# Performance work log

Hardware: AMD Instinct MI355X
Metric: run time of the kernel (lower is better)

The kernel has to match this reference:

```python
import jax, jax.numpy as jnp
import numpy as np

N_GENES = 2000
D_MODEL = 256
N_LAYERS = 4
D_STATE = 16
D_CONV = 4
EXPAND = 2
D_INNER = EXPAND * D_MODEL  # 512
DT_RANK = (D_MODEL + 15) // 16  # 16


def layer_norm(x, w, b, eps=1e-5):
    mu = jnp.mean(x, axis=-1, keepdims=True)
    var = jnp.mean((x - mu) ** 2, axis=-1, keepdims=True)
    return (x - mu) * jax.lax.rsqrt(var + eps) * w + b


def mamba_mixer(h, in_w, cw, cb, xp_w, dtp_w, dtp_b, A_log, Dvec, out_w):
    # h: [B, L, d_model]
    B, L, _ = h.shape
    xz = jnp.einsum('bld,ed->ble', h, in_w)            # [B,L,2*Di]
    u, z = jnp.split(xz, 2, axis=-1)                    # [B,L,Di] each
    # causal depthwise conv1d (kernel D_CONV)
    up = jnp.pad(u, ((0, 0), (D_CONV - 1, 0), (0, 0)))
    u = sum(up[:, k:k + L, :] * cw[:, k] for k in range(D_CONV)) + cb
    u = jax.nn.silu(u)
    # input-dependent dt, B, C
    xdbc = jnp.einsum('bld,ed->ble', u, xp_w)           # [B,L,dt_rank+2N]
    dt_r = xdbc[..., :DT_RANK]
    Bm = xdbc[..., DT_RANK:DT_RANK + D_STATE]           # [B,L,N]
    Cm = xdbc[..., DT_RANK + D_STATE:]                  # [B,L,N]
    dt = jax.nn.softplus(jnp.einsum('blr,dr->bld', dt_r, dtp_w) + dtp_b)  # [B,L,Di]
    A = -jnp.exp(A_log)                                 # [Di,N]
    dA = jnp.exp(dt[..., None] * A)                     # [B,L,Di,N]
    dBu = dt[..., None] * Bm[:, :, None, :] * u[..., None]

    def step(hst, inp):
        a, bu = inp
        hst = a * hst + bu
        return hst, hst

    h0 = jnp.zeros((B, D_INNER, D_STATE), dA.dtype)
    _, hs = jax.lax.scan(step, h0, (jnp.moveaxis(dA, 1, 0), jnp.moveaxis(dBu, 1, 0)))
    y = jnp.einsum('lbdn,lbn->bld', hs, jnp.moveaxis(Cm, 1, 0)) + u * Dvec
    y = y * jax.nn.silu(z)
    return jnp.einsum('bld,ed->ble', y, out_w)          # [B,L,d_model]


def setup_inputs() -> dict:
    key = jax.random.key(0)
    ks = jax.random.split(key, 16)
    nl = N_LAYERS
    inp = {
        'x': jax.random.normal(ks[0], (2, N_GENES), jnp.float32),
        'bulk_in_w': jax.random.normal(ks[1], (D_MODEL,), jnp.float32),
        'bulk_in_b': jnp.zeros((D_MODEL,), jnp.float32),
        'gene_emb': jax.random.normal(ks[2], (1, N_GENES, D_MODEL), jnp.float32) * 0.02,
        'mod_emb': jax.random.normal(ks[3], (1, 1, D_MODEL), jnp.float32) * 0.02,
        'ln_w': jnp.ones((nl, D_MODEL), jnp.float32),
        'ln_b': jnp.zeros((nl, D_MODEL), jnp.float32),
        'in_proj_w': jax.random.normal(ks[4], (nl, 2 * D_INNER, D_MODEL), jnp.float32) * (D_MODEL ** -0.5),
        'conv_w': jax.random.normal(ks[5], (nl, D_INNER, D_CONV), jnp.float32) * (D_CONV ** -0.5),
        'conv_b': jnp.zeros((nl, D_INNER), jnp.float32),
        'x_proj_w': jax.random.normal(ks[6], (nl, DT_RANK + 2 * D_STATE, D_INNER), jnp.float32) * (D_INNER ** -0.5),
        'dt_proj_w': jax.random.normal(ks[7], (nl, D_INNER, DT_RANK), jnp.float32) * 0.01,
        'dt_proj_b': jnp.full((nl, D_INNER), -4.0, jnp.float32),
        'A_log': jnp.broadcast_to(jnp.log(jnp.arange(1, D_STATE + 1, dtype=jnp.float32)), (nl, D_INNER, D_STATE)).copy(),
        'D': jnp.ones((nl, D_INNER), jnp.float32),
        'out_proj_w': jax.random.normal(ks[8], (nl, D_MODEL, D_INNER), jnp.float32) * (D_INNER ** -0.5),
        'fin_w': jnp.ones((D_MODEL,), jnp.float32),
        'fin_b': jnp.zeros((D_MODEL,), jnp.float32),
        'head_w': jax.random.normal(ks[9], (D_MODEL,), jnp.float32) * (D_MODEL ** -0.5),
        'head_b': jnp.zeros((), jnp.float32),
    }
    return inp


def reference(x, bulk_in_w, bulk_in_b, gene_emb, mod_emb, ln_w, ln_b, in_proj_w,
              conv_w, conv_b, x_proj_w, dt_proj_w, dt_proj_b, A_log, D, out_proj_w,
              fin_w, fin_b, head_w, head_b):
    # token embed (modality='bulk'); Linear(1,d_model) == x[...,None]*w + b
    h = x[..., None] * bulk_in_w + bulk_in_b + gene_emb + mod_emb  # [B,L,d_model]
    for i in range(N_LAYERS):
        h = h + mamba_mixer(layer_norm(h, ln_w[i], ln_b[i]), in_proj_w[i], conv_w[i],
                            conv_b[i], x_proj_w[i], dt_proj_w[i], dt_proj_b[i],
                            A_log[i], D[i], out_proj_w[i])
    h = layer_norm(h, fin_w, fin_b)
    y = jnp.einsum('bld,d->bl', h, head_w) + head_b  # bulk head, squeeze(-1)
    return y
```

## Files before the change

kernel.cpp:

```cpp
#include <hip/hip_runtime.h>
#include <math.h>

#define B_  2
#define L_  2000
#define DM_ 256
#define DI_ 512
#define DS_ 16
#define NL_ 4
#define BL_ (B_*L_)
#define BLP_ 4096
#define NC_  125
#define CL_  16
#define NST_ (B_*DI_*DS_)

#define NF_IP_ (NL_*64*8*64)
#define NF_OP_ (NL_*16*16*64)
#define NF_XP_ (NL_*3*16*64)
#define NF_TOT_ (NF_IP_ + NF_OP_ + NF_XP_)

typedef unsigned short ushort_t;
typedef __attribute__((ext_vector_type(8))) short bf16x8;
typedef __attribute__((ext_vector_type(4))) float f32x4;

__device__ __forceinline__ float siluf(float x) { return x / (1.f + __expf(-x)); }
__device__ __forceinline__ ushort_t f2bf(float x) {
    unsigned int u = __float_as_uint(x);
    return (ushort_t)((u + 0x7FFFu + ((u >> 16) & 1u)) >> 16);
}
__device__ __forceinline__ float bf2f(ushort_t v) {
    return __uint_as_float(((unsigned int)v) << 16);
}

__global__ __launch_bounds__(256) void embed_f2bf_kernel(
    const float* __restrict__ x, const float* __restrict__ biw,
    const float* __restrict__ bib, const float* __restrict__ ge,
    const float* __restrict__ me, const float* __restrict__ lnw,
    const float* __restrict__ lnb,
    float* __restrict__ h, ushort_t* __restrict__ aln,
    const float* __restrict__ ipw, const float* __restrict__ opw,
    const float* __restrict__ xpw, ushort_t* __restrict__ ipwb,
    ushort_t* __restrict__ opwb, ushort_t* __restrict__ xpwb)
{
    if (blockIdx.x < BL_) {
        __shared__ float sm[8];
        int bl = blockIdx.x, d = threadIdx.x;
        int l = bl % L_;
        float v = x[bl]*biw[d] + bib[d] + ge[(size_t)l*DM_ + d] + me[d];
        h[(size_t)bl*DM_ + d] = v;
        float s = v, q = v*v;
        #pragma unroll
        for (int o = 32; o > 0; o >>= 1) {
            s += __shfl_down(s, o);
            q += __shfl_down(q, o);
        }
        if ((d & 63) == 0) { sm[d >> 6] = s; sm[4 + (d >> 6)] = q; }
        __syncthreads();
        float sum = sm[0]+sm[1]+sm[2]+sm[3];
        float ssq = sm[4]+sm[5]+sm[6]+sm[7];
        float mu  = sum * (1.f/DM_);
        float inv = rsqrtf(fmaxf(ssq*(1.f/DM_) - mu*mu, 0.f) + 1e-5f);
        aln[(size_t)bl*DM_ + d] = f2bf((v - mu)*inv*lnw[d] + lnb[d]);
    } else {
        int i = (blockIdx.x - BL_)*256 + threadIdx.x;
        if (i >= NF_TOT_) return;
        const float* src; ushort_t* dst;
        if (i < NF_IP_) {
            int f = i;
            int li   = f >> 15;
            int r    = f & 32767;
            int t    = r >> 9;
            int rem  = r & 511;
            int ks   = rem >> 6;
            int lane = rem & 63;
            src = ipw + ((size_t)(li*1024 + t*16 + (lane & 15)))*DM_
                      + ks*32 + (lane >> 4)*8;
            dst = ipwb + (size_t)f*8;
        } else if (i < NF_IP_ + NF_OP_) {
            int f = i - NF_IP_;
            int li   = f >> 14;
            int r    = f & 16383;
            int t    = r >> 10;
            int rem  = r & 1023;
            int ks   = rem >> 6;
            int lane = rem & 63;
            src = opw + ((size_t)(li*256 + t*16 + (lane & 15)))*DI_
                      + ks*32 + (lane >> 4)*8;
            dst = opwb + (size_t)f*8;
        } else {
            int f = i - NF_IP_ - NF_OP_;
            int li   = f / 3072;
            int r    = f % 3072;
            int t    = r >> 10;
            int rem  = r & 1023;
            int ks   = rem >> 6;
            int lane = rem & 63;
            src = xpw + ((size_t)(li*48 + t*16 + (lane & 15)))*DI_
                      + ks*32 + (lane >> 4)*8;
            dst = xpwb + (size_t)f*8;
        }
        float4 v0 = *(const float4*)src;
        float4 v1 = *(const float4*)(src + 4);
        __align__(16) ushort_t o[8];
        o[0] = f2bf(v0.x); o[1] = f2bf(v0.y); o[2] = f2bf(v0.z); o[3] = f2bf(v0.w);
        o[4] = f2bf(v1.x); o[5] = f2bf(v1.y); o[6] = f2bf(v1.z); o[7] = f2bf(v1.w);
        *(uint4*)dst = *(const uint4*)o;
    }
}

__global__ __launch_bounds__(256) void gemm_bf(
    const ushort_t* __restrict__ A, const ushort_t* __restrict__ Wp,
    ushort_t* __restrict__ C)
{
    __shared__ ushort_t a_s[128*64];
    const int r0 = blockIdx.x*128, c0 = blockIdx.y*128;
    const int tid = threadIdx.x;
    const int lane = tid & 63, w = tid >> 6;
    const int wm = (w & 1)*64, wn = (w >> 1)*64;
    const int qd = lane >> 4, l16 = lane & 15;
    const int tb = (c0 + wn) >> 4;
    f32x4 acc[4][4] = {};
    for (int kc = 0; kc < DM_; kc += 64) {
        #pragma unroll
        for (int q = 0; q < 4; q++) {
            int ch = tid + 256*q;
            int row = ch >> 3, col8 = (ch & 7)*8;
            *(bf16x8*)&a_s[row*64 + col8] =
                *(const bf16x8*)(A + (size_t)(r0 + row)*DM_ + kc + col8);
        }
        __syncthreads();
        #pragma unroll
        for (int ks = 0; ks < 2; ks++) {
            int ksg = (kc >> 5) + ks;
            bf16x8 af[4], bf[4];
            #pragma unroll
            for (int i = 0; i < 4; i++)
                af[i] = *(const bf16x8*)&a_s[(wm + i*16 + l16)*64 + ks*32 + qd*8];
            #pragma unroll
            for (int j = 0; j < 4; j++)
                bf[j] = *(const bf16x8*)(Wp +
                    (((size_t)(tb + j)*8 + ksg)*64 + lane)*8);
            #pragma unroll
            for (int i = 0; i < 4; i++) {
                #pragma unroll
                for (int j = 0; j < 4; j++)
                    acc[i][j] = __builtin_amdgcn_mfma_f32_16x16x32_bf16(
                        af[i], bf[j], acc[i][j], 0, 0, 0);
            }
        }
        __syncthreads();
    }
    #pragma unroll
    for (int i = 0; i < 4; i++) {
        #pragma unroll
        for (int j = 0; j < 4; j++) {
            #pragma unroll
            for (int r = 0; r < 4; r++) {
                int row = r0 + wm + i*16 + qd*4 + r;
                int col = c0 + wn + j*16 + l16;
                C[(size_t)row*1024 + col] = f2bf(acc[i][j][r]);
            }
        }
    }
}

__global__ __launch_bounds__(512) void conv_xproj512(
    const ushort_t* __restrict__ xz, const float* __restrict__ cw,
    const float* __restrict__ cb, const ushort_t* __restrict__ XWp,
    const float* __restrict__ DTW, const float* __restrict__ DTB,
    const float* __restrict__ Alog,
    ushort_t* __restrict__ u_bf, float* __restrict__ bn,
    float* __restrict__ cn, ushort_t* __restrict__ dtn,
    float2* __restrict__ sa)
{
    __shared__ ushort_t xs[19][520];
    __shared__ ushort_t us[16][520];
    __shared__ float ps[8*768];
    __shared__ float dtr_s[16][16];
    const int c = blockIdx.x, b = blockIdx.y, l0 = c*CL_;
    const int tid = threadIdx.x;
    const int lane = tid & 63, w = tid >> 6;
    const int qd = lane >> 4, l16 = lane & 15;
    for (int f = tid; f < 19*64; f += 512) {
        int row = f >> 6, c8 = (f & 63)*8;
        int l = l0 - 3 + row;
        uint4 v = {0u,0u,0u,0u};
        if (l >= 0) v = *(const uint4*)(xz + (size_t)(b*L_ + l)*1024 + c8);
        *(uint4*)&xs[row][c8] = v;
    }
    __syncthreads();
    {
        int ch = tid;
        float4 wv = *(const float4*)(cw + ch*4);
        float bias = cb[ch];
        float x0 = bf2f(xs[0][ch]);
        float x1 = bf2f(xs[1][ch]);
        float x2 = bf2f(xs[2][ch]);
        #pragma unroll
        for (int j = 0; j < 16; j++) {
            float x3 = bf2f(xs[3 + j][ch]);
            float v = fmaf(x0, wv.x, fmaf(x1, wv.y, fmaf(x2, wv.z, fmaf(x3, wv.w, bias))));
            us[j][ch] = f2bf(siluf(v));
            x0 = x1; x1 = x2; x2 = x3;
        }
    }
    __syncthreads();
    for (int f = tid; f < 16*64; f += 512) {
        int row = f >> 6, c8 = (f & 63)*8;
        *(uint4*)(u_bf + (size_t)(b*L_ + l0 + row)*512 + c8) =
            *(const uint4*)&us[row][c8];
    }
    f32x4 acc[3] = {};
    #pragma unroll
    for (int st = 0; st < 2; st++) {
        int k = w*64 + st*32 + qd*8;
        int ksg = w*2 + st;
        bf16x8 af = *(const bf16x8*)&us[l16][k];
        #pragma unroll
        for (int j = 0; j < 3; j++) {
            bf16x8 bv = *(const bf16x8*)(XWp +
                (((size_t)j*16 + ksg)*64 + lane)*8);
            acc[j] = __builtin_amdgcn_mfma_f32_16x16x32_bf16(af, bv, acc[j], 0, 0, 0);
        }
    }
    #pragma unroll
    for (int j = 0; j < 3; j++)
        #pragma unroll
        for (int r = 0; r < 4; r++)
            ps[w*768 + (qd*4 + r)*48 + j*16 + l16] = acc[j][r];
    __syncthreads();
    for (int e = tid; e < 768; e += 512) {
        float v = ps[e] + ps[768+e] + ps[1536+e] + ps[2304+e]
                + ps[3072+e] + ps[3840+e] + ps[4608+e] + ps[5376+e];
        ps[e] = v;
    }
    __syncthreads();
    if (tid < 256) {
        int row = tid >> 4, n = tid & 15;
        dtr_s[row][n] = ps[row*48 + n];
        size_t base = ((size_t)(b*L_) + l0 + row)*DS_ + n;
        bn[base] = ps[row*48 + 16 + n];
        cn[base] = ps[row*48 + 32 + n];
    }
    __syncthreads();
    {
        const int d = tid;
        float wreg[16];
        const float4* wp = (const float4*)(DTW + (size_t)d*16);
        #pragma unroll
        for (int k4 = 0; k4 < 4; k4++) {
            float4 v = wp[k4];
            wreg[4*k4+0] = v.x; wreg[4*k4+1] = v.y;
            wreg[4*k4+2] = v.z; wreg[4*k4+3] = v.w;
        }
        float bias = DTB[d];
        float dtv[16];
        #pragma unroll
        for (int r = 0; r < 16; r++) {
            float a = bias;
            #pragma unroll
            for (int k = 0; k < 16; k++) a = fmaf(dtr_s[r][k], wreg[k], a);
            float dt = a > 20.f ? a : log1pf(__expf(a));
            ushort_t dtb16 = f2bf(dt);
            dtn[((size_t)(b*L_) + l0 + r)*DI_ + d] = dtb16;
            dtv[r] = bf2f(dtb16);
        }
        float Ac[DS_], s[DS_], ap[DS_];
        const float* ar = Alog + (size_t)d*DS_;
        #pragma unroll
        for (int n = 0; n < DS_; n++) { Ac[n] = -__expf(ar[n]); s[n] = 0.f; ap[n] = 1.f; }
        #pragma unroll
        for (int l = 0; l < 16; l++) {
            float dt = dtv[l];
            float u  = bf2f(us[l][d]);
            float dtu = dt*u;
            #pragma unroll
            for (int n = 0; n < DS_; n++) {
                float e = __expf(dt*Ac[n]);
                s[n] = fmaf(e, s[n], dtu*ps[l*48 + 16 + n]);
                ap[n] *= e;
            }
        }
        size_t ib = (((size_t)c*B_ + b)*DI_ + d)*DS_;
        float2* sap = sa + ib;
        #pragma unroll
        for (int k = 0; k < 8; k++)
            *(float4*)&sap[2*k] = make_float4(s[2*k], ap[2*k], s[2*k+1], ap[2*k+1]);
    }
}

__global__ __launch_bounds__(64) void scan_phase2(
    const float2* __restrict__ sa, float* __restrict__ sinc)
{
    const int t = blockIdx.x*64 + threadIdx.x;
    float s = 0.f;
    for (int g = 0; g < 5; g++) {
        float2 v[25];
        #pragma unroll
        for (int i = 0; i < 25; i++)
            v[i] = sa[(size_t)(g*25 + i)*NST_ + t];
        #pragma unroll
        for (int i = 0; i < 25; i++) {
            sinc[(size_t)(g*25 + i)*NST_ + t] = s;
            s = fmaf(v[i].y, s, v[i].x);
        }
    }
}

template<int LAST>
__global__ __launch_bounds__(512) void phase3_fused(
    const ushort_t* __restrict__ dtn, const ushort_t* __restrict__ u_bf,
    const float* __restrict__ bn, const float* __restrict__ cn,
    const float* __restrict__ Alog, const float* __restrict__ Dv,
    const float* __restrict__ sinc, const ushort_t* __restrict__ xz,
    const ushort_t* __restrict__ opw, float* __restrict__ h,
    const float* __restrict__ lnw, const float* __restrict__ lnb,
    const ushort_t* __restrict__ ipw, ushort_t* __restrict__ xz_out,
    const float* __restrict__ hw, const float* __restrict__ hb,
    float* __restrict__ out)
{
    __shared__ float b_sh[CL_*DS_];
    __shared__ float c_sh[CL_*DS_];
    __shared__ ushort_t ys[16][520];
    __shared__ union { ushort_t dt_t[16][520]; ushort_t z_t[16][520]; } T0;
    __shared__ union { ushort_t u_t[16][520];  ushort_t a_sh[16][264]; } T1;
    __shared__ float2 red2[128];
    __shared__ float2 muv[16];
    const int c = blockIdx.x, b = blockIdx.y, l0 = c*CL_;
    const int tid = threadIdx.x;
    const int w = tid >> 6, lane = tid & 63;
    const int qd = lane >> 4, l16 = lane & 15;
    {
        int f = tid & 255;
        size_t src = ((size_t)(b*L_) + l0)*DS_ + f;
        if (tid < 256) b_sh[f] = bn[src];
        else           c_sh[f] = cn[src];
    }
    {
        const int r = tid >> 5, cb16 = (tid & 31)*16;
        size_t rb = ((size_t)(b*L_) + l0 + r)*DI_ + cb16;
        *(uint4*)&T0.dt_t[r][cb16]     = *(const uint4*)(dtn + rb);
        *(uint4*)&T0.dt_t[r][cb16 + 8] = *(const uint4*)(dtn + rb + 8);
        *(uint4*)&T1.u_t[r][cb16]      = *(const uint4*)(u_bf + rb);
        *(uint4*)&T1.u_t[r][cb16 + 8]  = *(const uint4*)(u_bf + rb + 8);
    }
    const int d = tid;
    float Ac[DS_], s[DS_];
    {
        const float* ar = Alog + (size_t)d*DS_;
        #pragma unroll
        for (int n = 0; n < DS_; n++) Ac[n] = -__expf(ar[n]);
        size_t base = (((size_t)c*B_ + b)*DI_ + d)*DS_;
        #pragma unroll
        for (int n4 = 0; n4 < 4; n4++)
            *(float4*)&s[4*n4] = *(const float4*)(sinc + base + 4*n4);
    }
    const float Dd = Dv[d];
    __syncthreads();
    float y_reg[CL_];
    #pragma unroll
    for (int l = 0; l < CL_; l++) {
        float dt = bf2f(T0.dt_t[l][d]);
        float u  = bf2f(T1.u_t[l][d]);
        float dtu = dt*u;
        float y = u*Dd;
        #pragma unroll
        for (int n = 0; n < DS_; n++) {
            float e = __expf(dt*Ac[n]);
            s[n] = fmaf(e, s[n], dtu*b_sh[l*DS_ + n]);
            y = fmaf(s[n], c_sh[l*DS_ + n], y);
        }
        y_reg[l] = y;
    }
    __syncthreads();
    {
        const int r = tid >> 5, cb16 = (tid & 31)*16;
        size_t rb = ((size_t)(b*L_) + l0 + r)*1024 + 512 + cb16;
        *(uint4*)&T0.z_t[r][cb16]     = *(const uint4*)(xz + rb);
        *(uint4*)&T0.z_t[r][cb16 + 8] = *(const uint4*)(xz + rb + 8);
    }
    __syncthreads();
    #pragma unroll
    for (int l = 0; l < CL_; l++)
        ys[l][d] = f2bf(y_reg[l] * siluf(bf2f(T0.z_t[l][d])));
    __syncthreads();
    f32x4 acc[2] = {};
    #pragma unroll
    for (int ks = 0; ks < 16; ks++) {
        bf16x8 af = *(const bf16x8*)&ys[l16][ks*32 + qd*8];
        #pragma unroll
        for (int j = 0; j < 2; j++) {
            bf16x8 bv = *(const bf16x8*)(opw +
                (((size_t)(w*2 + j)*16 + ks)*64 + lane)*8);
            acc[j] = __builtin_amdgcn_mfma_f32_16x16x32_bf16(af, bv, acc[j], 0, 0, 0);
        }
    }
    float v[2][4];
    #pragma unroll
    for (int r = 0; r < 4; r++) {
        int lrow = qd*4 + r;
        size_t gr = (size_t)(b*L_ + l0 + lrow);
        float sm = 0.f, sq = 0.f;
        #pragma unroll
        for (int j = 0; j < 2; j++) {
            int col = w*32 + j*16 + l16;
            size_t idx = gr*DM_ + col;
            float vv = h[idx] + acc[j][r];
            if (!LAST) h[idx] = vv;
            v[j][r] = vv;
            sm += vv; sq += vv*vv;
        }
        sm += __shfl_xor(sm, 1); sq += __shfl_xor(sq, 1);
        sm += __shfl_xor(sm, 2); sq += __shfl_xor(sq, 2);
        sm += __shfl_xor(sm, 4); sq += __shfl_xor(sq, 4);
        sm += __shfl_xor(sm, 8); sq += __shfl_xor(sq, 8);
        if (l16 == 0) red2[w*16 + lrow] = make_float2(sm, sq);
    }
    __syncthreads();
    if (tid < 16) {
        float sm = 0.f, sq = 0.f;
        #pragma unroll
        for (int ww = 0; ww < 8; ww++) {
            float2 t = red2[ww*16 + tid];
            sm += t.x; sq += t.y;
        }
        float mu  = sm*(1.f/DM_);
        float inv = rsqrtf(fmaxf(sq*(1.f/DM_) - mu*mu, 0.f) + 1e-5f);
        muv[tid] = make_float2(mu, inv);
    }
    __syncthreads();
    if (!LAST) {
        #pragma unroll
        for (int r = 0; r < 4; r++) {
            int lrow = qd*4 + r;
            float2 mi = muv[lrow];
            #pragma unroll
            for (int j = 0; j < 2; j++) {
                int col = w*32 + j*16 + l16;
                T1.a_sh[lrow][col] = f2bf((v[j][r] - mi.x)*mi.y*lnw[col] + lnb[col]);
            }
        }
        __syncthreads();
        f32x4 acc2[8] = {};
        const int n0 = w*128;
        #pragma unroll
        for (int ks = 0; ks < 8; ks++) {
            bf16x8 af = *(const bf16x8*)&T1.a_sh[l16][ks*32 + qd*8];
            #pragma unroll
            for (int j2 = 0; j2 < 8; j2++) {
                bf16x8 bv = *(const bf16x8*)(ipw +
                    (((size_t)(w*8 + j2)*8 + ks)*64 + lane)*8);
                acc2[j2] = __builtin_amdgcn_mfma_f32_16x16x32_bf16(af, bv, acc2[j2], 0, 0, 0);
            }
        }
        #pragma unroll
        for (int j2 = 0; j2 < 8; j2++) {
            #pragma unroll
            for (int r = 0; r < 4; r++) {
                size_t row = (size_t)(b*L_ + l0 + qd*4 + r);
                xz_out[row*1024 + n0 + j2*16 + l16] = f2bf(acc2[j2][r]);
            }
        }
    } else {
        float hd[4];
        #pragma unroll
        for (int r = 0; r < 4; r++) {
            int lrow = qd*4 + r;
            float2 mi = muv[lrow];
            float aa = 0.f;
            #pragma unroll
            for (int j = 0; j < 2; j++) {
                int col = w*32 + j*16 + l16;
                float nv = (v[j][r] - mi.x)*mi.y*lnw[col] + lnb[col];
                aa = fmaf(nv, hw[col], aa);
            }
            hd[r] = aa;
        }
        #pragma unroll
        for (int r = 0; r < 4; r++) {
            float xv = hd[r];
            xv += __shfl_xor(xv, 1); xv += __shfl_xor(xv, 2);
            xv += __shfl_xor(xv, 4); xv += __shfl_xor(xv, 8);
            if (l16 == 0) red2[w*16 + qd*4 + r].x = xv;
        }
        __syncthreads();
        if (tid < 16) {
            float xv = 0.f;
            #pragma unroll
            for (int ww = 0; ww < 8; ww++) xv += red2[ww*16 + tid].x;
            out[(size_t)(b*L_) + l0 + tid] = xv + hb[0];
        }
    }
}

extern "C" void kernel_launch(void* const* d_in, const int* in_sizes, int n_in,
                              void* d_out, int out_size, void* d_ws, size_t ws_size,
                              hipStream_t stream)
{
    const float* x    = (const float*)d_in[0];
    const float* biw  = (const float*)d_in[1];
    const float* bib  = (const float*)d_in[2];
    const float* ge   = (const float*)d_in[3];
    const float* me   = (const float*)d_in[4];
    const float* lnw  = (const float*)d_in[5];
    const float* lnb  = (const float*)d_in[6];
    const float* ipw  = (const float*)d_in[7];
    const float* cw   = (const float*)d_in[8];
    const float* cb   = (const float*)d_in[9];
    const float* xpw  = (const float*)d_in[10];
    const float* dtw  = (const float*)d_in[11];
    const float* dtb  = (const float*)d_in[12];
    const float* alog = (const float*)d_in[13];
    const float* Dv   = (const float*)d_in[14];
    const float* opw  = (const float*)d_in[15];
    const float* fw   = (const float*)d_in[16];
    const float* fb   = (const float*)d_in[17];
    const float* hw   = (const float*)d_in[18];
    const float* hb   = (const float*)d_in[19];
    float* out = (float*)d_out;

    float* ws  = (float*)d_ws;
    float* h      = ws;
    float* bn     = h + (size_t)BLP_*DM_;
    float* cn     = bn + (size_t)B_*L_*DS_;
    float2* sa    = (float2*)(cn + (size_t)B_*L_*DS_);
    float* sinc   = (float*)(sa + (size_t)NC_*NST_);
    ushort_t* aln   = (ushort_t*)(sinc + (size_t)NC_*NST_);
    ushort_t* xz_bf = aln + (size_t)BLP_*DM_;
    ushort_t* u_bf  = xz_bf + (size_t)BLP_*1024;
    ushort_t* dtn   = u_bf + (size_t)BLP_*DI_;
    ushort_t* ipwb  = dtn + (size_t)B_*L_*DI_;
    ushort_t* opwb  = ipwb + (size_t)NL_*1024*DM_;
    ushort_t* xpwb  = opwb + (size_t)NL_*DM_*DI_;

    const int conv_blocks = (NF_TOT_ + 255)/256;
    embed_f2bf_kernel<<<BL_ + conv_blocks, 256, 0, stream>>>(
        x, biw, bib, ge, me, lnw, lnb, h, aln,
        ipw, opw, xpw, ipwb, opwb, xpwb);

    gemm_bf<<<dim3(BLP_/128, 1024/128), 256, 0, stream>>>(
        aln, ipwb, xz_bf);

    for (int i = 0; i < NL_; i++) {
        conv_xproj512<<<dim3(NC_, B_), 512, 0, stream>>>(
            xz_bf, cw + i*DI_*4, cb + i*DI_, xpwb + (size_t)i*48*512,
            dtw + (size_t)i*DI_*16, dtb + i*DI_, alog + (size_t)i*DI_*DS_,
            u_bf, bn, cn, dtn, sa);
        scan_phase2<<<NST_/64, 64, 0, stream>>>(sa, sinc);
        if (i < NL_-1) {
            phase3_fused<0><<<dim3(NC_, B_), 512, 0, stream>>>(
                dtn, u_bf, bn, cn, alog + (size_t)i*DI_*DS_, Dv + i*DI_,
                sinc, xz_bf, opwb + (size_t)i*DM_*DI_, h,
                lnw + (i+1)*DM_, lnb + (i+1)*DM_,
                ipwb + (size_t)(i+1)*1024*DM_, xz_bf,
                nullptr, nullptr, nullptr);
        } else {
            phase3_fused<1><<<dim3(NC_, B_), 512, 0, stream>>>(
                dtn, u_bf, bn, cn, alog + (size_t)i*DI_*DS_, Dv + i*DI_,
                sinc, xz_bf, opwb + (size_t)i*DM_*DI_, h,
                fw, fb,
                nullptr, xz_bf,
                hw, hb, out);
        }
    }
}
```

Baseline: 354.9 us.

## Fuse layer phase3 with next layer's conv/x-proj using halo recomputation

Merges each layer's output stage (scan finish, out-proj, residual, layernorm, in-proj) with the next layer's conv and x-projection into one kernel, removing one launch per layer boundary. Each block recomputes three halo rows of the previous chunk's scan so the causal conv can run locally. Buffers are ping-ponged across layers, and the xz buffer is split into separate u and z arrays. The cost is redundant scan and GEMM work for the halo rows, plus higher shared-memory and register pressure.

```diff
diff --git a/kernel.cpp b/kernel.cpp
--- a/kernel.cpp
+++ b/kernel.cpp
@@ -9,8 +9,8 @@
 #define NL_ 4
 #define BL_ (B_*L_)
 #define BLP_ 4096
+#define CL_  16
 #define NC_  125
-#define CL_  16
 #define NST_ (B_*DI_*DS_)
 
 #define NF_IP_ (NL_*64*8*64)
@@ -66,34 +66,25 @@
         const float* src; ushort_t* dst;
         if (i < NF_IP_) {
             int f = i;
-            int li   = f >> 15;
-            int r    = f & 32767;
-            int t    = r >> 9;
-            int rem  = r & 511;
-            int ks   = rem >> 6;
-            int lane = rem & 63;
+            int li = f >> 15, r = f & 32767;
+            int t = r >> 9, rem = r & 511;
+            int ks = rem >> 6, lane = rem & 63;
             src = ipw + ((size_t)(li*1024 + t*16 + (lane & 15)))*DM_
                       + ks*32 + (lane >> 4)*8;
             dst = ipwb + (size_t)f*8;
         } else if (i < NF_IP_ + NF_OP_) {
             int f = i - NF_IP_;
-            int li   = f >> 14;
-            int r    = f & 16383;
-            int t    = r >> 10;
-            int rem  = r & 1023;
-            int ks   = rem >> 6;
-            int lane = rem & 63;
+            int li = f >> 14, r = f & 16383;
+            int t = r >> 10, rem = r & 1023;
+            int ks = rem >> 6, lane = rem & 63;
             src = opw + ((size_t)(li*256 + t*16 + (lane & 15)))*DI_
                       + ks*32 + (lane >> 4)*8;
             dst = opwb + (size_t)f*8;
         } else {
             int f = i - NF_IP_ - NF_OP_;
-            int li   = f / 3072;
-            int r    = f % 3072;
-            int t    = r >> 10;
-            int rem  = r & 1023;
-            int ks   = rem >> 6;
-            int lane = rem & 63;
+            int li = f / 3072, r = f % 3072;
+            int t = r >> 10, rem = r & 1023;
+            int ks = rem >> 6, lane = rem & 63;
             src = xpw + ((size_t)(li*48 + t*16 + (lane & 15)))*DI_
                       + ks*32 + (lane >> 4)*8;
             dst = xpwb + (size_t)f*8;
@@ -109,7 +100,7 @@
 
 __global__ __launch_bounds__(256) void gemm_bf(
     const ushort_t* __restrict__ A, const ushort_t* __restrict__ Wp,
-    ushort_t* __restrict__ C)
+    ushort_t* __restrict__ XU, ushort_t* __restrict__ ZZ)
 {
     __shared__ ushort_t a_s[128*64];
     const int r0 = blockIdx.x*128, c0 = blockIdx.y*128;
@@ -157,18 +148,20 @@
             for (int r = 0; r < 4; r++) {
                 int row = r0 + wm + i*16 + qd*4 + r;
                 int col = c0 + wn + j*16 + l16;
-                C[(size_t)row*1024 + col] = f2bf(acc[i][j][r]);
+                ushort_t val = f2bf(acc[i][j][r]);
+                if (col < 512) XU[(size_t)row*512 + col] = val;
+                else           ZZ[(size_t)row*512 + col - 512] = val;
             }
         }
     }
 }
 
-__global__ __launch_bounds__(512) void conv_xproj512(
-    const ushort_t* __restrict__ xz, const float* __restrict__ cw,
+__global__ __launch_bounds__(512) void conv0(
+    const ushort_t* __restrict__ xu, const float* __restrict__ cw,
     const float* __restrict__ cb, const ushort_t* __restrict__ XWp,
     const float* __restrict__ DTW, const float* __restrict__ DTB,
     const float* __restrict__ Alog,
-    ushort_t* __restrict__ u_bf, float* __restrict__ bn,
+    ushort_t* __restrict__ u_o, float* __restrict__ bn,
     float* __restrict__ cn, ushort_t* __restrict__ dtn,
     float2* __restrict__ sa)
 {
@@ -184,7 +177,7 @@
         int row = f >> 6, c8 = (f & 63)*8;
         int l = l0 - 3 + row;
         uint4 v = {0u,0u,0u,0u};
-        if (l >= 0) v = *(const uint4*)(xz + (size_t)(b*L_ + l)*1024 + c8);
+        if (l >= 0) v = *(const uint4*)(xu + (size_t)(b*L_ + l)*512 + c8);
         *(uint4*)&xs[row][c8] = v;
     }
     __syncthreads();
@@ -206,7 +199,7 @@
     __syncthreads();
     for (int f = tid; f < 16*64; f += 512) {
         int row = f >> 6, c8 = (f & 63)*8;
-        *(uint4*)(u_bf + (size_t)(b*L_ + l0 + row)*512 + c8) =
+        *(uint4*)(u_o + (size_t)(b*L_ + l0 + row)*512 + c8) =
             *(const uint4*)&us[row][c8];
     }
     f32x4 acc[3] = {};
@@ -217,8 +210,7 @@
         bf16x8 af = *(const bf16x8*)&us[l16][k];
         #pragma unroll
         for (int j = 0; j < 3; j++) {
-            bf16x8 bv = *(const bf16x8*)(XWp +
-                (((size_t)j*16 + ksg)*64 + lane)*8);
+            bf16x8 bv = *(const bf16x8*)(XWp + (((size_t)j*16 + ksg)*64 + lane)*8);
             acc[j] = __builtin_amdgcn_mfma_f32_16x16x32_bf16(af, bv, acc[j], 0, 0, 0);
         }
     }
@@ -306,15 +298,397 @@
     }
 }
 
-template<int LAST>
-__global__ __launch_bounds__(512) void phase3_fused(
+__global__ __launch_bounds__(512) void fprime(
+    const ushort_t* __restrict__ dtn_p, const ushort_t* __restrict__ u_p,
+    const float* __restrict__ bn_p, const float* __restrict__ cn_p,
+    const float* __restrict__ alog_p, const float* __restrict__ Dv_p,
+    const float* __restrict__ sinc, const ushort_t* __restrict__ zz_p,
+    const ushort_t* __restrict__ opw_p,
+    const float* __restrict__ h_in, float* __restrict__ h_out,
+    const float* __restrict__ lnw_i, const float* __restrict__ lnb_i,
+    const ushort_t* __restrict__ ipw_i,
+    const float* __restrict__ cw_i, const float* __restrict__ cb_i,
+    const ushort_t* __restrict__ xpw_i,
+    const float* __restrict__ dtw_i, const float* __restrict__ dtb_i,
+    const float* __restrict__ alog_i,
+    ushort_t* __restrict__ u_o, float* __restrict__ bn_o,
+    float* __restrict__ cn_o, ushort_t* __restrict__ dtn_o,
+    float2* __restrict__ sa, ushort_t* __restrict__ zz_o)
+{
+    __shared__ __align__(16) char smem[57344];
+    __shared__ float2 red2[8*19];
+    __shared__ float2 muv[19];
+    ushort_t (*dt_t)[520] = (ushort_t(*)[520])(smem);
+    ushort_t (*u_t)[520]  = (ushort_t(*)[520])(smem + 16640);
+    float*    bc          = (float*)(smem + 33280);
+    ushort_t (*ys)[520]   = (ushort_t(*)[520])(smem);
+    ushort_t (*z_t)[520]  = (ushort_t(*)[520])(smem + 33280);
+    ushort_t (*a_sh)[264] = (ushort_t(*)[264])(smem);
+    ushort_t (*xs)[520]   = (ushort_t(*)[520])(smem + 16896);
+    ushort_t (*us)[520]   = (ushort_t(*)[520])(smem + 36656);
+    float*    ps          = (float*)(smem);
+    float    (*dtr)[16]   = (float(*)[16])(smem + 24576);
+    const int c = blockIdx.x, b = blockIdx.y, l0 = c*CL_;
+    const int tid = threadIdx.x;
+    const int w = tid >> 6, lane = tid & 63;
+    const int qd = lane >> 4, l16 = lane & 15;
+    const int d = tid;
+    float Ac[DS_];
+    {
+        const float* ar = alog_p + (size_t)d*DS_;
+        #pragma unroll
+        for (int n = 0; n < DS_; n++) Ac[n] = -__expf(ar[n]);
+    }
+    const float Dd = Dv_p[d];
+    float y_halo[3];
+    if (c > 0) {
+        {
+            const int r = tid >> 5, cb16 = (tid & 31)*16;
+            size_t rb = ((size_t)(b*L_) + l0 - 16 + r)*DI_ + cb16;
+            *(uint4*)&dt_t[r][cb16]     = *(const uint4*)(dtn_p + rb);
+            *(uint4*)&dt_t[r][cb16 + 8] = *(const uint4*)(dtn_p + rb + 8);
+            *(uint4*)&u_t[r][cb16]      = *(const uint4*)(u_p + rb);
+            *(uint4*)&u_t[r][cb16 + 8]  = *(const uint4*)(u_p + rb + 8);
+        }
+        {
+            int f = tid & 255;
+            size_t src = ((size_t)(b*L_) + l0 - 16)*DS_ + f;
+            if (tid < 256) bc[512 + f] = bn_p[src];
+            else           bc[768 + f] = cn_p[src];
+        }
+        float s[DS_];
+        {
+            size_t base = (((size_t)(c-1)*B_ + b)*DI_ + d)*DS_;
+            #pragma unroll
+            for (int n4 = 0; n4 < 4; n4++)
+                *(float4*)&s[4*n4] = *(const float4*)(sinc + base + 4*n4);
+        }
+        __syncthreads();
+        #pragma unroll
+        for (int l = 0; l < CL_; l++) {
+            float dt = bf2f(dt_t[l][d]);
+            float u  = bf2f(u_t[l][d]);
+            float dtu = dt*u;
+            float y = u*Dd;
+            #pragma unroll
+            for (int n = 0; n < DS_; n++) {
+                float e = __expf(dt*Ac[n]);
+                s[n] = fmaf(e, s[n], dtu*bc[512 + l*DS_ + n]);
+                y = fmaf(s[n], bc[768 + l*DS_ + n], y);
+            }
+            if (l >= 13) y_halo[l - 13] = y;
+        }
+        __syncthreads();
+    }
+    float y_reg[CL_];
+    {
+        {
+            const int r = tid >> 5, cb16 = (tid & 31)*16;
+            size_t rb = ((size_t)(b*L_) + l0 + r)*DI_ + cb16;
+            *(uint4*)&dt_t[r][cb16]     = *(const uint4*)(dtn_p + rb);
+            *(uint4*)&dt_t[r][cb16 + 8] = *(const uint4*)(dtn_p + rb + 8);
+            *(uint4*)&u_t[r][cb16]      = *(const uint4*)(u_p + rb);
+            *(uint4*)&u_t[r][cb16 + 8]  = *(const uint4*)(u_p + rb + 8);
+        }
+        {
+            int f = tid & 255;
+            size_t src = ((size_t)(b*L_) + l0)*DS_ + f;
+            if (tid < 256) bc[f]       = bn_p[src];
+            else           bc[256 + f] = cn_p[src];
+        }
+        float s[DS_];
+        {
+            size_t base = (((size_t)c*B_ + b)*DI_ + d)*DS_;
+            #pragma unroll
+            for (int n4 = 0; n4 < 4; n4++)
+                *(float4*)&s[4*n4] = *(const float4*)(sinc + base + 4*n4);
+        }
+        __syncthreads();
+        #pragma unroll
+        for (int l = 0; l < CL_; l++) {
+            float dt = bf2f(dt_t[l][d]);
+            float u  = bf2f(u_t[l][d]);
+            float dtu = dt*u;
+            float y = u*Dd;
+            #pragma unroll
+            for (int n = 0; n < DS_; n++) {
+                float e = __expf(dt*Ac[n]);
+                s[n] = fmaf(e, s[n], dtu*bc[l*DS_ + n]);
+                y = fmaf(s[n], bc[256 + l*DS_ + n], y);
+            }
+            y_reg[l] = y;
+        }
+        __syncthreads();
+    }
+    for (int f = tid; f < 19*32; f += 512) {
+        int r = f >> 5, cb16 = (f & 31)*16;
+        int grow = (r < 16) ? (l0 + r) : (l0 + r - 19);
+        uint4 v0 = {0u,0u,0u,0u}, v1 = {0u,0u,0u,0u};
+        if (grow >= 0) {
+            const ushort_t* p = zz_p + ((size_t)(b*L_) + grow)*512 + cb16;
+            v0 = *(const uint4*)p;
+            v1 = *(const uint4*)(p + 8);
+        }
+        *(uint4*)&z_t[r][cb16]     = v0;
+        *(uint4*)&z_t[r][cb16 + 8] = v1;
+    }
+    {
+        int zlo = (c > 0) ? 19 : 16;
+        for (int f = tid; f < (32 - zlo)*64; f += 512) {
+            int row = zlo + (f >> 6), c8 = (f & 63)*8;
+            uint4 zz4 = {0u,0u,0u,0u};
+            *(uint4*)&ys[row][c8] = zz4;
+        }
+    }
+    __syncthreads();
+    #pragma unroll
+    for (int l = 0; l < CL_; l++)
+        ys[l][d] = f2bf(y_reg[l] * siluf(bf2f(z_t[l][d])));
+    if (c > 0) {
+        #pragma unroll
+        for (int k = 0; k < 3; k++)
+            ys[16 + k][d] = f2bf(y_halo[k] * siluf(bf2f(z_t[16 + k][d])));
+    }
+    __syncthreads();
+    f32x4 acc[2][2] = {};
+    #pragma unroll
+    for (int ks = 0; ks < 16; ks++) {
+        bf16x8 af0 = *(const bf16x8*)&ys[l16][ks*32 + qd*8];
+        bf16x8 af1 = *(const bf16x8*)&ys[16 + l16][ks*32 + qd*8];
+        #pragma unroll
+        for (int j = 0; j < 2; j++) {
+            bf16x8 bv = *(const bf16x8*)(opw_p +
+                (((size_t)(w*2 + j)*16 + ks)*64 + lane)*8);
+            acc[0][j] = __builtin_amdgcn_mfma_f32_16x16x32_bf16(af0, bv, acc[0][j], 0, 0, 0);
+            acc[1][j] = __builtin_amdgcn_mfma_f32_16x16x32_bf16(af1, bv, acc[1][j], 0, 0, 0);
+        }
+    }
+    float v[2][4], vh[2][3];
+    #pragma unroll
+    for (int r = 0; r < 4; r++) {
+        int lrow = qd*4 + r;
+        size_t gr = (size_t)(b*L_ + l0 + lrow);
+        float sm = 0.f, sq = 0.f;
+        #pragma unroll
+        for (int j = 0; j < 2; j++) {
+            int col = w*32 + j*16 + l16;
+            float vv = h_in[gr*DM_ + col] + acc[0][j][r];
+            h_out[gr*DM_ + col] = vv;
+            v[j][r] = vv;
+            sm += vv; sq += vv*vv;
+        }
+        sm += __shfl_xor(sm, 1); sq += __shfl_xor(sq, 1);
+        sm += __shfl_xor(sm, 2); sq += __shfl_xor(sq, 2);
+        sm += __shfl_xor(sm, 4); sq += __shfl_xor(sq, 4);
+        sm += __shfl_xor(sm, 8); sq += __shfl_xor(sq, 8);
+        if (l16 == 0) red2[w*19 + lrow] = make_float2(sm, sq);
+    }
+    if (qd == 0) {
+        #pragma unroll
+        for (int r = 0; r < 3; r++) {
+            int grow = l0 - 3 + r; if (grow < 0) grow = 0;
+            size_t gr = (size_t)(b*L_ + grow);
+            float sm = 0.f, sq = 0.f;
+            #pragma unroll
+            for (int j = 0; j < 2; j++) {
+                int col = w*32 + j*16 + l16;
+                float vv = h_in[gr*DM_ + col] + acc[1][j][r];
+                vh[j][r] = vv;
+                sm += vv; sq += vv*vv;
+            }
+            sm += __shfl_xor(sm, 1); sq += __shfl_xor(sq, 1);
+            sm += __shfl_xor(sm, 2); sq += __shfl_xor(sq, 2);
+            sm += __shfl_xor(sm, 4); sq += __shfl_xor(sq, 4);
+            sm += __shfl_xor(sm, 8); sq += __shfl_xor(sq, 8);
+            if (l16 == 0) red2[w*19 + 16 + r] = make_float2(sm, sq);
+        }
+    }
+    __syncthreads();
+    if (tid < 19) {
+        float sm = 0.f, sq = 0.f;
+        #pragma unroll
+        for (int ww = 0; ww < 8; ww++) {
+            float2 t = red2[ww*19 + tid];
+            sm += t.x; sq += t.y;
+        }
+        float mu  = sm*(1.f/DM_);
+        float inv = rsqrtf(fmaxf(sq*(1.f/DM_) - mu*mu, 0.f) + 1e-5f);
+        muv[tid] = make_float2(mu, inv);
+    }
+    __syncthreads();
+    #pragma unroll
+    for (int r = 0; r < 4; r++) {
+        int lrow = qd*4 + r;
+        float2 mi = muv[lrow];
+        #pragma unroll
+        for (int j = 0; j < 2; j++) {
+            int col = w*32 + j*16 + l16;
+            a_sh[lrow][col] = f2bf((v[j][r] - mi.x)*mi.y*lnw_i[col] + lnb_i[col]);
+        }
+    }
+    if (qd == 0) {
+        #pragma unroll
+        for (int r = 0; r < 3; r++) {
+            float2 mi = muv[16 + r];
+            #pragma unroll
+            for (int j = 0; j < 2; j++) {
+                int col = w*32 + j*16 + l16;
+                a_sh[16 + r][col] = f2bf((vh[j][r] - mi.x)*mi.y*lnw_i[col] + lnb_i[col]);
+            }
+        }
+    }
+    for (int f = tid; f < 13*32; f += 512) {
+        int row = 19 + (f >> 5), c8 = (f & 31)*8;
+        uint4 zz4 = {0u,0u,0u,0u};
+        *(uint4*)&a_sh[row][c8] = zz4;
+    }
+    __syncthreads();
+    {
+        f32x4 acc2[2][8] = {};
+        const int n0 = w*128;
+        #pragma unroll
+        for (int ks = 0; ks < 8; ks++) {
+            bf16x8 af0 = *(const bf16x8*)&a_sh[l16][ks*32 + qd*8];
+            bf16x8 af1 = *(const bf16x8*)&a_sh[16 + l16][ks*32 + qd*8];
+            #pragma unroll
+            for (int j2 = 0; j2 < 8; j2++) {
+                bf16x8 bv = *(const bf16x8*)(ipw_i +
+                    (((size_t)(w*8 + j2)*8 + ks)*64 + lane)*8);
+                acc2[0][j2] = __builtin_amdgcn_mfma_f32_16x16x32_bf16(af0, bv, acc2[0][j2], 0, 0, 0);
+                acc2[1][j2] = __builtin_amdgcn_mfma_f32_16x16x32_bf16(af1, bv, acc2[1][j2], 0, 0, 0);
+            }
+        }
+        __syncthreads();
+        #pragma unroll
+        for (int j2 = 0; j2 < 8; j2++) {
+            #pragma unroll
+            for (int r = 0; r < 4; r++) {
+                int col = n0 + j2*16 + l16;
+                int lrow = qd*4 + r;
+                ushort_t val0 = f2bf(acc2[0][j2][r]);
+                if (col < 512) xs[3 + lrow][col] = val0;
+                else zz_o[((size_t)(b*L_) + l0 + lrow)*512 + col - 512] = val0;
+                if (qd == 0 && r < 3 && col < 512)
+                    xs[r][col] = f2bf(acc2[1][j2][r]);
+            }
+        }
+    }
+    if (c == 0) {
+        for (int f = tid; f < 3*64; f += 512) {
+            int row = f >> 6, c8 = (f & 63)*8;
+            uint4 zz4 = {0u,0u,0u,0u};
+            *(uint4*)&xs[row][c8] = zz4;
+        }
+    }
+    __syncthreads();
+    {
+        int ch = tid;
+        float4 wv = *(const float4*)(cw_i + ch*4);
+        float bias = cb_i[ch];
+        float x0 = bf2f(xs[0][ch]);
+        float x1 = bf2f(xs[1][ch]);
+        float x2 = bf2f(xs[2][ch]);
+        #pragma unroll
+        for (int j = 0; j < 16; j++) {
+            float x3 = bf2f(xs[3 + j][ch]);
+            float vv = fmaf(x0, wv.x, fmaf(x1, wv.y, fmaf(x2, wv.z, fmaf(x3, wv.w, bias))));
+            us[j][ch] = f2bf(siluf(vv));
+            x0 = x1; x1 = x2; x2 = x3;
+        }
+    }
+    __syncthreads();
+    for (int f = tid; f < 16*64; f += 512) {
+        int row = f >> 6, c8 = (f & 63)*8;
+        *(uint4*)(u_o + (size_t)(b*L_ + l0 + row)*512 + c8) =
+            *(const uint4*)&us[row][c8];
+    }
+    {
+        f32x4 accx[3] = {};
+        #pragma unroll
+        for (int st = 0; st < 2; st++) {
+            int k = w*64 + st*32 + qd*8;
+            int ksg = w*2 + st;
+            bf16x8 af = *(const bf16x8*)&us[l16][k];
+            #pragma unroll
+            for (int j = 0; j < 3; j++) {
+                bf16x8 bv = *(const bf16x8*)(xpw_i + (((size_t)j*16 + ksg)*64 + lane)*8);
+                accx[j] = __builtin_amdgcn_mfma_f32_16x16x32_bf16(af, bv, accx[j], 0, 0, 0);
+            }
+        }
+        __syncthreads();
+        #pragma unroll
+        for (int j = 0; j < 3; j++)
+            #pragma unroll
+            for (int r = 0; r < 4; r++)
+                ps[w*768 + (qd*4 + r)*48 + j*16 + l16] = accx[j][r];
+    }
+    __syncthreads();
+    for (int e = tid; e < 768; e += 512) {
+        float vv = ps[e] + ps[768+e] + ps[1536+e] + ps[2304+e]
+                 + ps[3072+e] + ps[3840+e] + ps[4608+e] + ps[5376+e];
+        ps[e] = vv;
+    }
+    __syncthreads();
+    if (tid < 256) {
+        int row = tid >> 4, n = tid & 15;
+        dtr[row][n] = ps[row*48 + n];
+        size_t base = ((size_t)(b*L_) + l0 + row)*DS_ + n;
+        bn_o[base] = ps[row*48 + 16 + n];
+        cn_o[base] = ps[row*48 + 32 + n];
+    }
+    __syncthreads();
+    {
+        float wreg[16];
+        const float4* wp = (const float4*)(dtw_i + (size_t)d*16);
+        #pragma unroll
+        for (int k4 = 0; k4 < 4; k4++) {
+            float4 vv = wp[k4];
+            wreg[4*k4+0] = vv.x; wreg[4*k4+1] = vv.y;
+            wreg[4*k4+2] = vv.z; wreg[4*k4+3] = vv.w;
+        }
+        float bias = dtb_i[d];
+        float dtv[16];
+        #pragma unroll
+        for (int r = 0; r < 16; r++) {
+            float a = bias;
+            #pragma unroll
+            for (int k = 0; k < 16; k++) a = fmaf(dtr[r][k], wreg[k], a);
+            float dt = a > 20.f ? a : log1pf(__expf(a));
+            ushort_t dtb16 = f2bf(dt);
+            dtn_o[((size_t)(b*L_) + l0 + r)*DI_ + d] = dtb16;
+            dtv[r] = bf2f(dtb16);
+        }
+        float Ai[DS_], s[DS_], ap[DS_];
+        const float* ar = alog_i + (size_t)d*DS_;
+        #pragma unroll
+        for (int n = 0; n < DS_; n++) { Ai[n] = -__expf(ar[n]); s[n] = 0.f; ap[n] = 1.f; }
+        #pragma unroll
+        for (int l = 0; l < 16; l++) {
+            float dt = dtv[l];
+            float u  = bf2f(us[l][d]);
+            float dtu = dt*u;
+            #pragma unroll
+            for (int n = 0; n < DS_; n++) {
+                float e = __expf(dt*Ai[n]);
+                s[n] = fmaf(e, s[n], dtu*ps[l*48 + 16 + n]);
+                ap[n] *= e;
+            }
+        }
+        size_t ib = (((size_t)c*B_ + b)*DI_ + d)*DS_;
+        float2* sap = sa + ib;
+        #pragma unroll
+        for (int k = 0; k < 8; k++)
+            *(float4*)&sap[2*k] = make_float4(s[2*k], ap[2*k], s[2*k+1], ap[2*k+1]);
+    }
+}
+
+__global__ __launch_bounds__(512) void phase3_head(
     const ushort_t* __restrict__ dtn, const ushort_t* __restrict__ u_bf,
     const float* __restrict__ bn, const float* __restrict__ cn,
     const float* __restrict__ Alog, const float* __restrict__ Dv,
-    const float* __restrict__ sinc, const ushort_t* __restrict__ xz,
-    const ushort_t* __restrict__ opw, float* __restrict__ h,
-    const float* __restrict__ lnw, const float* __restrict__ lnb,
-    const ushort_t* __restrict__ ipw, ushort_t* __restrict__ xz_out,
+    const float* __restrict__ sinc, const ushort_t* __restrict__ zz,
+    const ushort_t* __restrict__ opw, const float* __restrict__ h,
+    const float* __restrict__ fw, const float* __restrict__ fb,
     const float* __restrict__ hw, const float* __restrict__ hb,
     float* __restrict__ out)
 {
@@ -322,7 +696,7 @@
     __shared__ float c_sh[CL_*DS_];
     __shared__ ushort_t ys[16][520];
     __shared__ union { ushort_t dt_t[16][520]; ushort_t z_t[16][520]; } T0;
-    __shared__ union { ushort_t u_t[16][520];  ushort_t a_sh[16][264]; } T1;
+    __shared__ ushort_t u_t[16][520];
     __shared__ float2 red2[128];
     __shared__ float2 muv[16];
     const int c = blockIdx.x, b = blockIdx.y, l0 = c*CL_;
@@ -340,8 +714,8 @@
         size_t rb = ((size_t)(b*L_) + l0 + r)*DI_ + cb16;
         *(uint4*)&T0.dt_t[r][cb16]     = *(const uint4*)(dtn + rb);
         *(uint4*)&T0.dt_t[r][cb16 + 8] = *(const uint4*)(dtn + rb + 8);
-        *(uint4*)&T1.u_t[r][cb16]      = *(const uint4*)(u_bf + rb);
-        *(uint4*)&T1.u_t[r][cb16 + 8]  = *(const uint4*)(u_bf + rb + 8);
+        *(uint4*)&u_t[r][cb16]         = *(const uint4*)(u_bf + rb);
+        *(uint4*)&u_t[r][cb16 + 8]     = *(const uint4*)(u_bf + rb + 8);
     }
     const int d = tid;
     float Ac[DS_], s[DS_];
@@ -360,7 +734,7 @@
     #pragma unroll
     for (int l = 0; l < CL_; l++) {
         float dt = bf2f(T0.dt_t[l][d]);
-        float u  = bf2f(T1.u_t[l][d]);
+        float u  = bf2f(u_t[l][d]);
         float dtu = dt*u;
         float y = u*Dd;
         #pragma unroll
@@ -374,9 +748,9 @@
     __syncthreads();
     {
         const int r = tid >> 5, cb16 = (tid & 31)*16;
-        size_t rb = ((size_t)(b*L_) + l0 + r)*1024 + 512 + cb16;
-        *(uint4*)&T0.z_t[r][cb16]     = *(const uint4*)(xz + rb);
-        *(uint4*)&T0.z_t[r][cb16 + 8] = *(const uint4*)(xz + rb + 8);
+        size_t rb = ((size_t)(b*L_) + l0 + r)*512 + cb16;
+        *(uint4*)&T0.z_t[r][cb16]     = *(const uint4*)(zz + rb);
+        *(uint4*)&T0.z_t[r][cb16 + 8] = *(const uint4*)(zz + rb + 8);
     }
     __syncthreads();
     #pragma unroll
@@ -403,9 +777,7 @@
         #pragma unroll
         for (int j = 0; j < 2; j++) {
             int col = w*32 + j*16 + l16;
-            size_t idx = gr*DM_ + col;
-            float vv = h[idx] + acc[j][r];
-            if (!LAST) h[idx] = vv;
+            float vv = h[gr*DM_ + col] + acc[j][r];
             v[j][r] = vv;
             sm += vv; sq += vv*vv;
         }
@@ -428,67 +800,33 @@
         muv[tid] = make_float2(mu, inv);
     }
     __syncthreads();
-    if (!LAST) {
-        #pragma unroll
-        for (int r = 0; r < 4; r++) {
-            int lrow = qd*4 + r;
-            float2 mi = muv[lrow];
-            #pragma unroll
-            for (int j = 0; j < 2; j++) {
-                int col = w*32 + j*16 + l16;
-                T1.a_sh[lrow][col] = f2bf((v[j][r] - mi.x)*mi.y*lnw[col] + lnb[col]);
-            }
-        }
-        __syncthreads();
-        f32x4 acc2[8] = {};
-        const int n0 = w*128;
-        #pragma unroll
-        for (int ks = 0; ks < 8; ks++) {
-            bf16x8 af = *(const bf16x8*)&T1.a_sh[l16][ks*32 + qd*8];
-            #pragma unroll
-            for (int j2 = 0; j2 < 8; j2++) {
-                bf16x8 bv = *(const bf16x8*)(ipw +
-                    (((size_t)(w*8 + j2)*8 + ks)*64 + lane)*8);
-                acc2[j2] = __builtin_amdgcn_mfma_f32_16x16x32_bf16(af, bv, acc2[j2], 0, 0, 0);
-            }
-        }
-        #pragma unroll
-        for (int j2 = 0; j2 < 8; j2++) {
-            #pragma unroll
-            for (int r = 0; r < 4; r++) {
-                size_t row = (size_t)(b*L_ + l0 + qd*4 + r);
-                xz_out[row*1024 + n0 + j2*16 + l16] = f2bf(acc2[j2][r]);
-            }
-        }
-    } else {
-        float hd[4];
-        #pragma unroll
-        for (int r = 0; r < 4; r++) {
-            int lrow = qd*4 + r;
-            float2 mi = muv[lrow];
-            float aa = 0.f;
-            #pragma unroll
-            for (int j = 0; j < 2; j++) {
-                int col = w*32 + j*16 + l16;
-                float nv = (v[j][r] - mi.x)*mi.y*lnw[col] + lnb[col];
-                aa = fmaf(nv, hw[col], aa);
-            }
-            hd[r] = aa;
-        }
-        #pragma unroll
-        for (int r = 0; r < 4; r++) {
-            float xv = hd[r];
-            xv += __shfl_xor(xv, 1); xv += __shfl_xor(xv, 2);
-            xv += __shfl_xor(xv, 4); xv += __shfl_xor(xv, 8);
-            if (l16 == 0) red2[w*16 + qd*4 + r].x = xv;
-        }
-        __syncthreads();
-        if (tid < 16) {
-            float xv = 0.f;
-            #pragma unroll
-            for (int ww = 0; ww < 8; ww++) xv += red2[ww*16 + tid].x;
-            out[(size_t)(b*L_) + l0 + tid] = xv + hb[0];
-        }
+    float hd[4];
+    #pragma unroll
+    for (int r = 0; r < 4; r++) {
+        int lrow = qd*4 + r;
+        float2 mi = muv[lrow];
+        float aa = 0.f;
+        #pragma unroll
+        for (int j = 0; j < 2; j++) {
+            int col = w*32 + j*16 + l16;
+            float nv = (v[j][r] - mi.x)*mi.y*fw[col] + fb[col];
+            aa = fmaf(nv, hw[col], aa);
+        }
+        hd[r] = aa;
+    }
+    #pragma unroll
+    for (int r = 0; r < 4; r++) {
+        float xv = hd[r];
+        xv += __shfl_xor(xv, 1); xv += __shfl_xor(xv, 2);
+        xv += __shfl_xor(xv, 4); xv += __shfl_xor(xv, 8);
+        if (l16 == 0) red2[w*16 + qd*4 + r].x = xv;
+    }
+    __syncthreads();
+    if (tid < 16) {
+        float xv = 0.f;
+        #pragma unroll
+        for (int ww = 0; ww < 8; ww++) xv += red2[ww*16 + tid].x;
+        out[(size_t)(b*L_) + l0 + tid] = xv + hb[0];
     }
 }
 
@@ -519,47 +857,63 @@
     float* out = (float*)d_out;
 
     float* ws  = (float*)d_ws;
-    float* h      = ws;
-    float* bn     = h + (size_t)BLP_*DM_;
-    float* cn     = bn + (size_t)B_*L_*DS_;
-    float2* sa    = (float2*)(cn + (size_t)B_*L_*DS_);
+    float* h0     = ws;
+    float* h1     = h0 + (size_t)BLP_*DM_;
+    float* bn0    = h1 + (size_t)BLP_*DM_;
+    float* cn0    = bn0 + (size_t)B_*L_*DS_;
+    float* bn1    = cn0 + (size_t)B_*L_*DS_;
+    float* cn1    = bn1 + (size_t)B_*L_*DS_;
+    float2* sa    = (float2*)(cn1 + (size_t)B_*L_*DS_);
     float* sinc   = (float*)(sa + (size_t)NC_*NST_);
-    ushort_t* aln   = (ushort_t*)(sinc + (size_t)NC_*NST_);
-    ushort_t* xz_bf = aln + (size_t)BLP_*DM_;
-    ushort_t* u_bf  = xz_bf + (size_t)BLP_*1024;
-    ushort_t* dtn   = u_bf + (size_t)BLP_*DI_;
-    ushort_t* ipwb  = dtn + (size_t)B_*L_*DI_;
-    ushort_t* opwb  = ipwb + (size_t)NL_*1024*DM_;
-    ushort_t* xpwb  = opwb + (size_t)NL_*DM_*DI_;
+    ushort_t* aln = (ushort_t*)(sinc + (size_t)NC_*NST_);
+    ushort_t* xu  = aln + (size_t)BLP_*DM_;
+    ushort_t* zz0 = xu  + (size_t)BLP_*512;
+    ushort_t* zz1 = zz0 + (size_t)BLP_*512;
+    ushort_t* u0  = zz1 + (size_t)BLP_*512;
+    ushort_t* u1  = u0  + (size_t)BLP_*512;
+    ushort_t* dt0 = u1  + (size_t)BLP_*512;
+    ushort_t* dt1 = dt0 + (size_t)BLP_*512;
+    ushort_t* ipwb = dt1 + (size_t)BLP_*512;
+    ushort_t* opwb = ipwb + (size_t)NF_IP_*8/NL_*NL_;
+    ushort_t* xpwb = opwb + (size_t)NF_OP_*8;
+
+    float* hbuf[2] = { h0, h1 };
+    float* bnb[2] = { bn0, bn1 };
+    float* cnb[2] = { cn0, cn1 };
+    ushort_t* zzb[2] = { zz0, zz1 };
+    ushort_t* ub[2]  = { u0, u1 };
+    ushort_t* dtnb[2] = { dt0, dt1 };
 
     const int conv_blocks = (NF_TOT_ + 255)/256;
     embed_f2bf_kernel<<<BL_ + conv_blocks, 256, 0, stream>>>(
-        x, biw, bib, ge, me, lnw, lnb, h, aln,
+        x, biw, bib, ge, me, lnw, lnb, h0, aln,
         ipw, opw, xpw, ipwb, opwb, xpwb);
 
     gemm_bf<<<dim3(BLP_/128, 1024/128), 256, 0, stream>>>(
-        aln, ipwb, xz_bf);
-
-    for (int i = 0; i < NL_; i++) {
-        conv_xproj512<<<dim3(NC_, B_), 512, 0, stream>>>(
-            xz_bf, cw + i*DI_*4, cb + i*DI_, xpwb + (size_t)i*48*512,
+        aln, ipwb, xu, zz0);
+
+    conv0<<<dim3(NC_, B_), 512, 0, stream>>>(
+        xu, cw, cb, xpwb, dtw, dtb, alog,
+        u0, bn0, cn0, dt0, sa);
+    scan_phase2<<<NST_/64, 64, 0, stream>>>(sa, sinc);
+
+    for (int i = 1; i < NL_; i++) {
+        int p = (i-1) & 1, q = i & 1;
+        fprime<<<dim3(NC_, B_), 512, 0, stream>>>(
+            dtnb[p], ub[p], bnb[p], cnb[p],
+            alog + (size_t)(i-1)*DI_*DS_, Dv + (i-1)*DI_,
+            sinc, zzb[p], opwb + (size_t)(i-1)*16*16*64*8,
+            hbuf[p], hbuf[q],
+            lnw + i*DM_, lnb + i*DM_, ipwb + (size_t)i*64*8*64*8,
+            cw + i*DI_*4, cb + i*DI_, xpwb + (size_t)i*3*16*64*8,
             dtw + (size_t)i*DI_*16, dtb + i*DI_, alog + (size_t)i*DI_*DS_,
-            u_bf, bn, cn, dtn, sa);
+            ub[q], bnb[q], cnb[q], dtnb[q], sa, zzb[q]);
         scan_phase2<<<NST_/64, 64, 0, stream>>>(sa, sinc);
-        if (i < NL_-1) {
-            phase3_fused<0><<<dim3(NC_, B_), 512, 0, stream>>>(
-                dtn, u_bf, bn, cn, alog + (size_t)i*DI_*DS_, Dv + i*DI_,
-                sinc, xz_bf, opwb + (size_t)i*DM_*DI_, h,
-                lnw + (i+1)*DM_, lnb + (i+1)*DM_,
-                ipwb + (size_t)(i+1)*1024*DM_, xz_bf,
-                nullptr, nullptr, nullptr);
-        } else {
-            phase3_fused<1><<<dim3(NC_, B_), 512, 0, stream>>>(
-                dtn, u_bf, bn, cn, alog + (size_t)i*DI_*DS_, Dv + i*DI_,
-                sinc, xz_bf, opwb + (size_t)i*DM_*DI_, h,
-                fw, fb,
-                nullptr, xz_bf,
-                hw, hb, out);
-        }
-    }
+    }
+
+    phase3_head<<<dim3(NC_, B_), 512, 0, stream>>>(
+        dtnb[1], ub[1], bnb[1], cnb[1],
+        alog + (size_t)3*DI_*DS_, Dv + 3*DI_,
+        sinc, zzb[1], opwb + (size_t)3*16*16*64*8, hbuf[1],
+        fw, fb, hw, hb, out);
 }
```

Measured after the change: 377.7 us. 1.06x slower.
